# Optimization experiments

Hardware: AMD Instinct MI355X
Metric: run time of the kernel (lower is better)

## Reference

```python
import jax, jax.numpy as jnp
import numpy as np

VOCAB = 32000
H = 256        # d_model
L = 4096       # l_max
N = 64         # SSM state size (S4 default)
CH = 1         # channels
BATCH = 8
PAD = 0        # pad_token_id
DT_MIN, DT_MAX = 0.001, 0.1


def setup_inputs() -> dict:
    key = jax.random.key(0)
    ks = jax.random.split(key, 8)
    input_ids = jax.random.randint(ks[0], (BATCH, L), 0, VOCAB)
    embedding = (jax.random.normal(ks[1], (VOCAB, H), dtype=jnp.float32) * 0.02).at[PAD].set(0.0)
    # S4D-Lin style initialization
    log_dt = jnp.log(DT_MIN) + jax.random.uniform(ks[2], (H,), dtype=jnp.float32) * (np.log(DT_MAX) - np.log(DT_MIN))
    A_log_re = jnp.full((H, N), np.log(0.5), dtype=jnp.float32)          # A_real = -exp(A_log_re)
    A_im = jnp.broadcast_to(np.pi * jnp.arange(N, dtype=jnp.float32), (H, N)).copy()
    B_re = jnp.ones((H, N), dtype=jnp.float32)
    B_im = jnp.zeros((H, N), dtype=jnp.float32)
    # bidirectional => 2*CH output channels for C
    C_re = jax.random.normal(ks[3], (2 * CH, H, N), dtype=jnp.float32) * (0.5 ** 0.5)
    C_im = jax.random.normal(ks[4], (2 * CH, H, N), dtype=jnp.float32) * (0.5 ** 0.5)
    D = jax.random.normal(ks[5], (CH, H), dtype=jnp.float32)
    W_out = jax.random.normal(ks[6], (2 * H, CH * H), dtype=jnp.float32) / np.sqrt(CH * H)
    b_out = jnp.zeros((2 * H,), dtype=jnp.float32)
    return {"input_ids": input_ids, "embedding": embedding, "log_dt": log_dt,
            "A_log_re": A_log_re, "A_im": A_im, "B_re": B_re, "B_im": B_im,
            "C_re": C_re, "C_im": C_im, "D": D, "W_out": W_out, "b_out": b_out}


def _s4_forward(input_ids, embedding, log_dt, A_log_re, A_im, B_re, B_im, C_re, C_im, D, W_out, b_out):
    u = embedding[input_ids]                 # (B, L, H) embedding lookup
    u = jnp.swapaxes(u, 1, 2)                # (B, H, L) transposed=True
    dt = jnp.exp(log_dt)                     # (H,)
    A = -jnp.exp(A_log_re) + 1j * A_im       # (H, N) Hurwitz diagonal SSM
    dtA = dt[:, None] * A                    # (H, N)
    dA = jnp.exp(dtA)                        # discrete A (ZOH)
    dB = (B_re + 1j * B_im) * (dA - 1.0) / A # discrete B (ZOH), (H, N)
    Cc = C_re + 1j * C_im                    # (2*CH, H, N)
    # Vandermonde kernel: K[c,h,l] = 2*Re(sum_n C[c,h,n] dB[h,n] exp(dtA[h,n]*l))
    pos = jnp.arange(L, dtype=jnp.float32)
    vand = jnp.exp(dtA[:, :, None] * pos)    # (H, N, L) complex
    K = 2.0 * jnp.einsum('chn,hn,hnl->chl', Cc, dB, vand).real  # (2*CH, H, L)
    # bidirectional: causal kernel + flipped anti-causal kernel, conv length 2L
    k0, k1 = K[:CH], K[CH:]
    k = jnp.pad(k0, ((0, 0), (0, 0), (0, L))) + jnp.pad(k1[..., ::-1], ((0, 0), (0, 0), (L, 0)))
    k_f = jnp.fft.rfft(k, n=2 * L)           # (CH, H, L+1)
    u_f = jnp.fft.rfft(u, n=2 * L)           # (B, H, L+1)
    y = jnp.fft.irfft(u_f[:, None] * k_f[None], n=2 * L)[..., :L]  # (B, CH, H, L)
    y = y + u[:, None, :, :] * D[None, :, :, None]                 # skip connection
    y = y.reshape(u.shape[0], CH * H, L)
    y = jax.nn.gelu(y, approximate=False)
    z = jnp.einsum('oi,bil->bol', W_out, y) + b_out[None, :, None]  # (B, 2H, L)
    y = z[:, :H] * jax.nn.sigmoid(z[:, H:])                          # GLU
    y = jnp.swapaxes(y, 1, 2)                # (B, L, H)
    return y[:, -1]                           # pool='last' -> (B, H)


def reference(input_ids, embedding, log_dt, A_log_re, A_im, B_re, B_im, C_re, C_im, D, W_out, b_out):
    return _s4_forward(input_ids, embedding, log_dt, A_log_re, A_im, B_re, B_im, C_re, C_im, D, W_out, b_out)
```

## Files before the change

### kernel.cpp

```cpp
#include <hip/hip_runtime.h>
#include <math.h>

#define HH 256
#define NN 64
#define LL 4096
#define BB 8


__global__ __launch_bounds__(512) void frontend_kernel(
    const int* __restrict__ ids, const float* __restrict__ emb,
    const float* __restrict__ log_dt, const float* __restrict__ A_log_re,
    const float* __restrict__ A_im, const float* __restrict__ B_re,
    const float* __restrict__ B_im, const float* __restrict__ C_re,
    const float* __restrict__ C_im,
    float* __restrict__ u_ws, float* __restrict__ Krev) {
    __shared__ union {
        struct { int ids_s[64]; float tb[2][64][65]; } a;
        struct { float powR[64][65]; float powI[64][65];
                 float2 dAt[64]; float2 e64t[64]; float2 W2[8][64]; } k;
    } sm;
    int t = threadIdx.x;
    if (blockIdx.x < BB * 64) {
        int b = blockIdx.x >> 6;
        int tile = blockIdx.x & 63;
        int w = t >> 6;
        int lane = t & 63;
        int rq = lane >> 4;
        int k = lane & 15;
        if (t < 64) sm.a.ids_s[t] = ids[b * LL + tile * 64 + t];
        __syncthreads();
        {
            int r0 = w * 8 + rq;
            float4 v0 = *(const float4*)(emb + (long)sm.a.ids_s[r0] * HH + 4 * k);
            float4 v1 = *(const float4*)(emb + (long)sm.a.ids_s[r0 + 4] * HH + 4 * k);
            sm.a.tb[0][r0][4 * k + 0] = v0.x;
            sm.a.tb[0][r0][4 * k + 1] = v0.y;
            sm.a.tb[0][r0][4 * k + 2] = v0.z;
            sm.a.tb[0][r0][4 * k + 3] = v0.w;
            sm.a.tb[0][r0 + 4][4 * k + 0] = v1.x;
            sm.a.tb[0][r0 + 4][4 * k + 1] = v1.y;
            sm.a.tb[0][r0 + 4][4 * k + 2] = v1.z;
            sm.a.tb[0][r0 + 4][4 * k + 3] = v1.w;
        }
        __syncthreads();
        #pragma unroll
        for (int c4 = 0; c4 < 4; ++c4) {
            int cur = c4 & 1;
            float4 v0, v1;
            if (c4 < 3) {
                int r0 = w * 8 + rq;
                v0 = *(const float4*)(emb + (long)sm.a.ids_s[r0] * HH +
                                      (c4 + 1) * 64 + 4 * k);
                v1 = *(const float4*)(emb + (long)sm.a.ids_s[r0 + 4] * HH +
                                      (c4 + 1) * 64 + 4 * k);
            }
            #pragma unroll
            for (int it = 0; it < 2; ++it) {
                int hq = w * 8 + it * 4 + rq;
                int s0 = 4 * k;
                float4 o;
                o.x = sm.a.tb[cur][s0 + 0][hq];
                o.y = sm.a.tb[cur][s0 + 1][hq];
                o.z = sm.a.tb[cur][s0 + 2][hq];
                o.w = sm.a.tb[cur][s0 + 3][hq];
                *(float4*)(u_ws + ((long)(b * HH + c4 * 64 + hq)) * LL +
                           tile * 64 + s0) = o;
            }
            if (c4 < 3) {
                int r0 = w * 8 + rq;
                sm.a.tb[cur ^ 1][r0][4 * k + 0] = v0.x;
                sm.a.tb[cur ^ 1][r0][4 * k + 1] = v0.y;
                sm.a.tb[cur ^ 1][r0][4 * k + 2] = v0.z;
                sm.a.tb[cur ^ 1][r0][4 * k + 3] = v0.w;
                sm.a.tb[cur ^ 1][r0 + 4][4 * k + 0] = v1.x;
                sm.a.tb[cur ^ 1][r0 + 4][4 * k + 1] = v1.y;
                sm.a.tb[cur ^ 1][r0 + 4][4 * k + 2] = v1.z;
                sm.a.tb[cur ^ 1][r0 + 4][4 * k + 3] = v1.w;
            }
            __syncthreads();
        }
    } else {
        int h = blockIdx.x - BB * 64;
        int w = __builtin_amdgcn_readfirstlane(t >> 6);
        int lane = t & 63;
        if (t < NN) {
            int n = t;
            int idx = h * NN + n;
            float dt = expf(log_dt[h]);
            float Are = -expf(A_log_re[idx]);
            float Aim = A_im[idx];
            float ea = expf(dt * Are);
            float sn, cs;
            sincosf(dt * Aim, &sn, &cs);
            float dAre = ea * cs, dAim = ea * sn;
            float numre = dAre - 1.0f, numim = dAim;
            float den = Are * Are + Aim * Aim;
            float qre = (numre * Are + numim * Aim) / den;
            float qim = (numim * Are - numre * Aim) / den;
            float bre = B_re[idx], bim = B_im[idx];
            float dBre = bre * qre - bim * qim;
            float dBim = bre * qim + bim * qre;
            float cre = C_re[idx], cim = C_im[idx];
            float wre = 2.0f * (cre * dBre - cim * dBim);
            float wim = 2.0f * (cre * dBim + cim * dBre);
            sm.k.dAt[n] = make_float2(dAre, dAim);
            float pr = dAre, pi = dAim;
            #pragma unroll
            for (int kq = 0; kq < 6; ++kq) {
                float nr = pr * pr - pi * pi;
                pi = 2.0f * pr * pi; pr = nr;
            }
            sm.k.e64t[n] = make_float2(pr, pi);
            #pragma unroll
            for (int kq = 0; kq < 3; ++kq) {
                float nr = pr * pr - pi * pi;
                pi = 2.0f * pr * pi; pr = nr;
            }
            float qr2 = wre, qi2 = wim;
            #pragma unroll
            for (int kk = 0; kk < 8; ++kk) {
                sm.k.W2[kk][n] = make_float2(qr2, qi2);
                float nr = qr2 * pr - qi2 * pi, ni = qr2 * pi + qi2 * pr;
                qr2 = nr; qi2 = ni;
            }
        }
        __syncthreads();
        {
            float2 a = sm.k.dAt[lane];
            float br = a.x, bi = a.y;
            #pragma unroll
            for (int kq = 0; kq < 3; ++kq) {
                float nr = br * br - bi * bi;
                bi = 2.0f * br * bi; br = nr;
            }
            float pr = 1.0f, pi = 0.0f;
            #pragma unroll
            for (int bit = 0; bit < 3; ++bit) {
                if ((w >> bit) & 1) {
                    float tr = pr * br - pi * bi;
                    pi = pr * bi + pi * br; pr = tr;
                }
                float t2 = br * br - bi * bi;
                bi = 2.0f * br * bi; br = t2;
            }
            #pragma unroll
            for (int i = 0; i < 8; ++i) {
                sm.k.powR[8 * w + i][lane] = pr;
                sm.k.powI[8 * w + i][lane] = pi;
                float tr = pr * a.x - pi * a.y;
                pi = pr * a.y + pi * a.x; pr = tr;
            }
        }
        __syncthreads();
        float kacc[8];
        #pragma unroll
        for (int j = 0; j < 8; ++j) kacc[j] = 0.0f;
        #pragma unroll 2
        for (int n = 0; n < NN; ++n) {
            float Pr = sm.k.powR[lane][n];
            float Pi = sm.k.powI[lane][n];
            float2 E = sm.k.e64t[n];
            float2 Wn = sm.k.W2[w][n];
            float vr = Wn.x * Pr - Wn.y * Pi;
            float vi = Wn.x * Pi + Wn.y * Pr;
            #pragma unroll
            for (int j = 0; j < 8; ++j) {
                kacc[j] += vr;
                float tr = vr * E.x - vi * E.y;
                vi = vr * E.y + vi * E.x; vr = tr;
            }
        }
        #pragma unroll
        for (int j = 0; j < 8; ++j) {
            int l = w * 512 + j * 64 + lane;
            Krev[h * LL + (LL - 1 - l)] = kacc[j];
        }
    }
}

__global__ __launch_bounds__(256) void conv_kernel(
    const float* __restrict__ u_ws, const float* __restrict__ Krev,
    const float* __restrict__ Dv, float* __restrict__ g) {
    __shared__ float partial[4];
    int t = threadIdx.x;
    int bh = blockIdx.x;
    int h = bh & (HH - 1);
    const float4* up = (const float4*)(u_ws + (long)bh * LL);
    const float4* kp = (const float4*)(Krev + h * LL);
    float acc = 0.0f;
    #pragma unroll
    for (int i = 0; i < 4; ++i) {
        float4 uv = up[i * 256 + t];
        float4 kv = kp[i * 256 + t];
        acc += uv.x * kv.x + uv.y * kv.y + uv.z * kv.z + uv.w * kv.w;
    }
    #pragma unroll
    for (int m = 32; m > 0; m >>= 1) acc += __shfl_xor(acc, m);
    if ((t & 63) == 0) partial[t >> 6] = acc;
    __syncthreads();
    if (t == 0) {
        float y = partial[0] + partial[1] + partial[2] + partial[3]
                + u_ws[(long)bh * LL + LL - 1] * Dv[h];
        float ge = 0.5f * y * (1.0f + erff(y * 0.70710678118654752f));
        g[bh] = ge;
    }
}

__global__ __launch_bounds__(256) void out_kernel(
    const float* __restrict__ g, const float* __restrict__ W,
    const float* __restrict__ bvec, float* __restrict__ out) {
    int b = blockIdx.x >> 7;
    int tile = blockIdx.x & 127;
    int t = threadIdx.x;
    int w = t >> 6, lane = t & 63;
    __shared__ float gs[HH];
    __shared__ float zb[4];
    gs[t] = g[b * HH + t];
    __syncthreads();
    int hh = tile * 2 + (w >> 1);
    int o = (w & 1) * HH + hh;
    float4 wv4 = ((const float4*)(W + o * HH))[lane];
    float4 gv4 = ((const float4*)gs)[lane];
    float p = wv4.x * gv4.x + wv4.y * gv4.y + wv4.z * gv4.z + wv4.w * gv4.w;
    #pragma unroll
    for (int m = 32; m > 0; m >>= 1) p += __shfl_xor(p, m);
    if (lane == 0) zb[w] = p + bvec[o];
    __syncthreads();
    if (t < 2) {
        int hq = tile * 2 + t;
        float z1 = zb[t * 2 + 0];
        float z2 = zb[t * 2 + 1];
        out[b * HH + hq] = z1 * (1.0f / (1.0f + expf(-z2)));
    }
}

extern "C" void kernel_launch(void* const* d_in, const int* in_sizes, int n_in,
                              void* d_out, int out_size, void* d_ws, size_t ws_size,
                              hipStream_t stream) {
    const int* input_ids = (const int*)d_in[0];
    const float* embedding = (const float*)d_in[1];
    const float* log_dt = (const float*)d_in[2];
    const float* A_log_re = (const float*)d_in[3];
    const float* A_im = (const float*)d_in[4];
    const float* B_re = (const float*)d_in[5];
    const float* B_im = (const float*)d_in[6];
    const float* C_re = (const float*)d_in[7];
    const float* C_im = (const float*)d_in[8];
    const float* D = (const float*)d_in[9];
    const float* W_out = (const float*)d_in[10];
    const float* b_out = (const float*)d_in[11];
    float* out = (float*)d_out;

    float* ws = (float*)d_ws;
    float* u_ws = ws + 327680;
    float* g = ws + 10813440;
    float* Krev = ws + 10815488;

    frontend_kernel<<<BB * 64 + HH, 512, 0, stream>>>(
        input_ids, embedding, log_dt, A_log_re, A_im, B_re, B_im, C_re, C_im,
        u_ws, Krev);

    conv_kernel<<<BB * HH, 256, 0, stream>>>(u_ws, Krev, D, g);

    out_kernel<<<BB * 128, 256, 0, stream>>>(g, W_out, b_out, out);
}
```

Baseline: 119.4 us.

## Gather embeddings directly in conv instead of materializing transposed u

Removes the separate embedding-gather-and-transpose pass that wrote the full (B,H,L) activation tensor to workspace. The K kernel is now stored time-major, and a new conv kernel gathers embedding rows by token id, multiplying them against K tiles loaded into LDS through async global-to-LDS loads, then writes per-chunk partial sums. The output kernel reduces those partials and fuses the skip term, GELU, projection and GLU, using one block per batch element. This cuts a large intermediate write and re-read, in exchange for a serialized K-generation stage ahead of the conv and a small grid in the final kernel.

```diff
diff --git a/kernel.cpp b/kernel.cpp
--- a/kernel.cpp
+++ b/kernel.cpp
@@ -5,232 +5,196 @@
 #define NN 64
 #define LL 4096
 #define BB 8
-
-
-__global__ __launch_bounds__(512) void frontend_kernel(
-    const int* __restrict__ ids, const float* __restrict__ emb,
+#define TK 32
+#define NCH (LL / TK)
+
+
+__global__ __launch_bounds__(512) void kmat_kernel(
     const float* __restrict__ log_dt, const float* __restrict__ A_log_re,
     const float* __restrict__ A_im, const float* __restrict__ B_re,
     const float* __restrict__ B_im, const float* __restrict__ C_re,
-    const float* __restrict__ C_im,
-    float* __restrict__ u_ws, float* __restrict__ Krev) {
-    __shared__ union {
-        struct { int ids_s[64]; float tb[2][64][65]; } a;
-        struct { float powR[64][65]; float powI[64][65];
-                 float2 dAt[64]; float2 e64t[64]; float2 W2[8][64]; } k;
-    } sm;
+    const float* __restrict__ C_im, float* __restrict__ Ktrev) {
+    __shared__ struct {
+        float powR[64][65]; float powI[64][65];
+        float2 dAt[64]; float2 e64t[64]; float2 W2[8][64];
+    } sk;
     int t = threadIdx.x;
-    if (blockIdx.x < BB * 64) {
-        int b = blockIdx.x >> 6;
-        int tile = blockIdx.x & 63;
-        int w = t >> 6;
-        int lane = t & 63;
-        int rq = lane >> 4;
-        int k = lane & 15;
-        if (t < 64) sm.a.ids_s[t] = ids[b * LL + tile * 64 + t];
-        __syncthreads();
-        {
-            int r0 = w * 8 + rq;
-            float4 v0 = *(const float4*)(emb + (long)sm.a.ids_s[r0] * HH + 4 * k);
-            float4 v1 = *(const float4*)(emb + (long)sm.a.ids_s[r0 + 4] * HH + 4 * k);
-            sm.a.tb[0][r0][4 * k + 0] = v0.x;
-            sm.a.tb[0][r0][4 * k + 1] = v0.y;
-            sm.a.tb[0][r0][4 * k + 2] = v0.z;
-            sm.a.tb[0][r0][4 * k + 3] = v0.w;
-            sm.a.tb[0][r0 + 4][4 * k + 0] = v1.x;
-            sm.a.tb[0][r0 + 4][4 * k + 1] = v1.y;
-            sm.a.tb[0][r0 + 4][4 * k + 2] = v1.z;
-            sm.a.tb[0][r0 + 4][4 * k + 3] = v1.w;
-        }
-        __syncthreads();
-        #pragma unroll
-        for (int c4 = 0; c4 < 4; ++c4) {
-            int cur = c4 & 1;
-            float4 v0, v1;
-            if (c4 < 3) {
-                int r0 = w * 8 + rq;
-                v0 = *(const float4*)(emb + (long)sm.a.ids_s[r0] * HH +
-                                      (c4 + 1) * 64 + 4 * k);
-                v1 = *(const float4*)(emb + (long)sm.a.ids_s[r0 + 4] * HH +
-                                      (c4 + 1) * 64 + 4 * k);
+    int h = blockIdx.x;
+    int w = __builtin_amdgcn_readfirstlane(t >> 6);
+    int lane = t & 63;
+    if (t < NN) {
+        int n = t;
+        int idx = h * NN + n;
+        float dt = expf(log_dt[h]);
+        float Are = -expf(A_log_re[idx]);
+        float Aim = A_im[idx];
+        float ea = expf(dt * Are);
+        float sn, cs;
+        sincosf(dt * Aim, &sn, &cs);
+        float dAre = ea * cs, dAim = ea * sn;
+        float numre = dAre - 1.0f, numim = dAim;
+        float den = Are * Are + Aim * Aim;
+        float qre = (numre * Are + numim * Aim) / den;
+        float qim = (numim * Are - numre * Aim) / den;
+        float bre = B_re[idx], bim = B_im[idx];
+        float dBre = bre * qre - bim * qim;
+        float dBim = bre * qim + bim * qre;
+        float cre = C_re[idx], cim = C_im[idx];
+        float wre = 2.0f * (cre * dBre - cim * dBim);
+        float wim = 2.0f * (cre * dBim + cim * dBre);
+        sk.dAt[n] = make_float2(dAre, dAim);
+        float pr = dAre, pi = dAim;
+        #pragma unroll
+        for (int kq = 0; kq < 6; ++kq) {
+            float nr = pr * pr - pi * pi;
+            pi = 2.0f * pr * pi; pr = nr;
+        }
+        sk.e64t[n] = make_float2(pr, pi);
+        #pragma unroll
+        for (int kq = 0; kq < 3; ++kq) {
+            float nr = pr * pr - pi * pi;
+            pi = 2.0f * pr * pi; pr = nr;
+        }
+        float qr2 = wre, qi2 = wim;
+        #pragma unroll
+        for (int kk = 0; kk < 8; ++kk) {
+            sk.W2[kk][n] = make_float2(qr2, qi2);
+            float nr = qr2 * pr - qi2 * pi, ni = qr2 * pi + qi2 * pr;
+            qr2 = nr; qi2 = ni;
+        }
+    }
+    __syncthreads();
+    {
+        float2 a = sk.dAt[lane];
+        float br = a.x, bi = a.y;
+        #pragma unroll
+        for (int kq = 0; kq < 3; ++kq) {
+            float nr = br * br - bi * bi;
+            bi = 2.0f * br * bi; br = nr;
+        }
+        float pr = 1.0f, pi = 0.0f;
+        #pragma unroll
+        for (int bit = 0; bit < 3; ++bit) {
+            if ((w >> bit) & 1) {
+                float tr = pr * br - pi * bi;
+                pi = pr * bi + pi * br; pr = tr;
             }
-            #pragma unroll
-            for (int it = 0; it < 2; ++it) {
-                int hq = w * 8 + it * 4 + rq;
-                int s0 = 4 * k;
-                float4 o;
-                o.x = sm.a.tb[cur][s0 + 0][hq];
-                o.y = sm.a.tb[cur][s0 + 1][hq];
-                o.z = sm.a.tb[cur][s0 + 2][hq];
-                o.w = sm.a.tb[cur][s0 + 3][hq];
-                *(float4*)(u_ws + ((long)(b * HH + c4 * 64 + hq)) * LL +
-                           tile * 64 + s0) = o;
-            }
-            if (c4 < 3) {
-                int r0 = w * 8 + rq;
-                sm.a.tb[cur ^ 1][r0][4 * k + 0] = v0.x;
-                sm.a.tb[cur ^ 1][r0][4 * k + 1] = v0.y;
-                sm.a.tb[cur ^ 1][r0][4 * k + 2] = v0.z;
-                sm.a.tb[cur ^ 1][r0][4 * k + 3] = v0.w;
-                sm.a.tb[cur ^ 1][r0 + 4][4 * k + 0] = v1.x;
-                sm.a.tb[cur ^ 1][r0 + 4][4 * k + 1] = v1.y;
-                sm.a.tb[cur ^ 1][r0 + 4][4 * k + 2] = v1.z;
-                sm.a.tb[cur ^ 1][r0 + 4][4 * k + 3] = v1.w;
-            }
-            __syncthreads();
-        }
-    } else {
-        int h = blockIdx.x - BB * 64;
-        int w = __builtin_amdgcn_readfirstlane(t >> 6);
-        int lane = t & 63;
-        if (t < NN) {
-            int n = t;
-            int idx = h * NN + n;
-            float dt = expf(log_dt[h]);
-            float Are = -expf(A_log_re[idx]);
-            float Aim = A_im[idx];
-            float ea = expf(dt * Are);
-            float sn, cs;
-            sincosf(dt * Aim, &sn, &cs);
-            float dAre = ea * cs, dAim = ea * sn;
-            float numre = dAre - 1.0f, numim = dAim;
-            float den = Are * Are + Aim * Aim;
-            float qre = (numre * Are + numim * Aim) / den;
-            float qim = (numim * Are - numre * Aim) / den;
-            float bre = B_re[idx], bim = B_im[idx];
-            float dBre = bre * qre - bim * qim;
-            float dBim = bre * qim + bim * qre;
-            float cre = C_re[idx], cim = C_im[idx];
-            float wre = 2.0f * (cre * dBre - cim * dBim);
-            float wim = 2.0f * (cre * dBim + cim * dBre);
-            sm.k.dAt[n] = make_float2(dAre, dAim);
-            float pr = dAre, pi = dAim;
-            #pragma unroll
-            for (int kq = 0; kq < 6; ++kq) {
-                float nr = pr * pr - pi * pi;
-                pi = 2.0f * pr * pi; pr = nr;
-            }
-            sm.k.e64t[n] = make_float2(pr, pi);
-            #pragma unroll
-            for (int kq = 0; kq < 3; ++kq) {
-                float nr = pr * pr - pi * pi;
-                pi = 2.0f * pr * pi; pr = nr;
-            }
-            float qr2 = wre, qi2 = wim;
-            #pragma unroll
-            for (int kk = 0; kk < 8; ++kk) {
-                sm.k.W2[kk][n] = make_float2(qr2, qi2);
-                float nr = qr2 * pr - qi2 * pi, ni = qr2 * pi + qi2 * pr;
-                qr2 = nr; qi2 = ni;
-            }
-        }
-        __syncthreads();
-        {
-            float2 a = sm.k.dAt[lane];
-            float br = a.x, bi = a.y;
-            #pragma unroll
-            for (int kq = 0; kq < 3; ++kq) {
-                float nr = br * br - bi * bi;
-                bi = 2.0f * br * bi; br = nr;
-            }
-            float pr = 1.0f, pi = 0.0f;
-            #pragma unroll
-            for (int bit = 0; bit < 3; ++bit) {
-                if ((w >> bit) & 1) {
-                    float tr = pr * br - pi * bi;
-                    pi = pr * bi + pi * br; pr = tr;
-                }
-                float t2 = br * br - bi * bi;
-                bi = 2.0f * br * bi; br = t2;
-            }
-            #pragma unroll
-            for (int i = 0; i < 8; ++i) {
-                sm.k.powR[8 * w + i][lane] = pr;
-                sm.k.powI[8 * w + i][lane] = pi;
-                float tr = pr * a.x - pi * a.y;
-                pi = pr * a.y + pi * a.x; pr = tr;
-            }
-        }
-        __syncthreads();
-        float kacc[8];
-        #pragma unroll
-        for (int j = 0; j < 8; ++j) kacc[j] = 0.0f;
-        #pragma unroll 2
-        for (int n = 0; n < NN; ++n) {
-            float Pr = sm.k.powR[lane][n];
-            float Pi = sm.k.powI[lane][n];
-            float2 E = sm.k.e64t[n];
-            float2 Wn = sm.k.W2[w][n];
-            float vr = Wn.x * Pr - Wn.y * Pi;
-            float vi = Wn.x * Pi + Wn.y * Pr;
-            #pragma unroll
-            for (int j = 0; j < 8; ++j) {
-                kacc[j] += vr;
-                float tr = vr * E.x - vi * E.y;
-                vi = vr * E.y + vi * E.x; vr = tr;
-            }
-        }
+            float t2 = br * br - bi * bi;
+            bi = 2.0f * br * bi; br = t2;
+        }
+        #pragma unroll
+        for (int i = 0; i < 8; ++i) {
+            sk.powR[8 * w + i][lane] = pr;
+            sk.powI[8 * w + i][lane] = pi;
+            float tr = pr * a.x - pi * a.y;
+            pi = pr * a.y + pi * a.x; pr = tr;
+        }
+    }
+    __syncthreads();
+    float kacc[8];
+    #pragma unroll
+    for (int j = 0; j < 8; ++j) kacc[j] = 0.0f;
+    #pragma unroll 2
+    for (int n = 0; n < NN; ++n) {
+        float Pr = sk.powR[lane][n];
+        float Pi = sk.powI[lane][n];
+        float2 E = sk.e64t[n];
+        float2 Wn = sk.W2[w][n];
+        float vr = Wn.x * Pr - Wn.y * Pi;
+        float vi = Wn.x * Pi + Wn.y * Pr;
         #pragma unroll
         for (int j = 0; j < 8; ++j) {
-            int l = w * 512 + j * 64 + lane;
-            Krev[h * LL + (LL - 1 - l)] = kacc[j];
-        }
-    }
-}
-
-__global__ __launch_bounds__(256) void conv_kernel(
-    const float* __restrict__ u_ws, const float* __restrict__ Krev,
-    const float* __restrict__ Dv, float* __restrict__ g) {
-    __shared__ float partial[4];
+            kacc[j] += vr;
+            float tr = vr * E.x - vi * E.y;
+            vi = vr * E.y + vi * E.x; vr = tr;
+        }
+    }
+    #pragma unroll
+    for (int j = 0; j < 8; ++j) {
+        int l = w * 512 + j * 64 + lane;
+        Ktrev[(long)(LL - 1 - l) * HH + h] = kacc[j];
+    }
+}
+
+__global__ __launch_bounds__(256) void gconv_kernel(
+    const int* __restrict__ ids, const float* __restrict__ emb,
+    const float* __restrict__ Ktrev, float* __restrict__ ypart) {
+    __shared__ float Kls[TK * HH];
+    __shared__ int idsl[TK];
     int t = threadIdx.x;
-    int bh = blockIdx.x;
-    int h = bh & (HH - 1);
-    const float4* up = (const float4*)(u_ws + (long)bh * LL);
-    const float4* kp = (const float4*)(Krev + h * LL);
+    int b = blockIdx.x >> 7;
+    int c = blockIdx.x & (NCH - 1);
+    int i0 = c * TK;
+    int wv = t >> 6, lane = t & 63;
+    if (t < TK) idsl[t] = ids[b * LL + i0 + t];
+    {
+        const float* src = Ktrev + (long)i0 * HH;
+        #pragma unroll
+        for (int r = 0; r < 8; ++r) {
+            int row = wv * 8 + r;
+            __builtin_amdgcn_global_load_lds(
+                (const __attribute__((address_space(1))) void*)
+                    (src + row * HH + lane * 4),
+                (__attribute__((address_space(3))) void*)(&Kls[row * HH]),
+                16, 0, 0);
+        }
+    }
+    __syncthreads();
     float acc = 0.0f;
-    #pragma unroll
-    for (int i = 0; i < 4; ++i) {
-        float4 uv = up[i * 256 + t];
-        float4 kv = kp[i * 256 + t];
-        acc += uv.x * kv.x + uv.y * kv.y + uv.z * kv.z + uv.w * kv.w;
-    }
-    #pragma unroll
-    for (int m = 32; m > 0; m >>= 1) acc += __shfl_xor(acc, m);
-    if ((t & 63) == 0) partial[t >> 6] = acc;
-    __syncthreads();
-    if (t == 0) {
-        float y = partial[0] + partial[1] + partial[2] + partial[3]
-                + u_ws[(long)bh * LL + LL - 1] * Dv[h];
-        float ge = 0.5f * y * (1.0f + erff(y * 0.70710678118654752f));
-        g[bh] = ge;
-    }
-}
-
-__global__ __launch_bounds__(256) void out_kernel(
-    const float* __restrict__ g, const float* __restrict__ W,
-    const float* __restrict__ bvec, float* __restrict__ out) {
-    int b = blockIdx.x >> 7;
-    int tile = blockIdx.x & 127;
+    #pragma unroll 8
+    for (int l = 0; l < TK; ++l) {
+        int id = idsl[l];
+        float v = emb[(long)id * HH + t];
+        acc = fmaf(v, Kls[l * HH + t], acc);
+    }
+    ypart[((long)(b * NCH + c)) * HH + t] = acc;
+}
+
+__global__ __launch_bounds__(512) void out_kernel(
+    const float* __restrict__ ypart, const int* __restrict__ ids,
+    const float* __restrict__ emb, const float* __restrict__ Dv,
+    const float* __restrict__ W, const float* __restrict__ bvec,
+    float* __restrict__ out) {
+    __shared__ float red[8][HH];
+    __shared__ float gs[HH];
+    __shared__ float zb[2 * HH];
     int t = threadIdx.x;
-    int w = t >> 6, lane = t & 63;
-    __shared__ float gs[HH];
-    __shared__ float zb[4];
-    gs[t] = g[b * HH + t];
-    __syncthreads();
-    int hh = tile * 2 + (w >> 1);
-    int o = (w & 1) * HH + hh;
-    float4 wv4 = ((const float4*)(W + o * HH))[lane];
-    float4 gv4 = ((const float4*)gs)[lane];
-    float p = wv4.x * gv4.x + wv4.y * gv4.y + wv4.z * gv4.z + wv4.w * gv4.w;
-    #pragma unroll
-    for (int m = 32; m > 0; m >>= 1) p += __shfl_xor(p, m);
-    if (lane == 0) zb[w] = p + bvec[o];
-    __syncthreads();
-    if (t < 2) {
-        int hq = tile * 2 + t;
-        float z1 = zb[t * 2 + 0];
-        float z2 = zb[t * 2 + 1];
-        out[b * HH + hq] = z1 * (1.0f / (1.0f + expf(-z2)));
+    int b = blockIdx.x;
+    int wv = t >> 6, lane = t & 63;
+    float4 s4 = make_float4(0.f, 0.f, 0.f, 0.f);
+    const float4* yp4 = (const float4*)(ypart + (long)b * NCH * HH);
+    #pragma unroll 4
+    for (int cc = 0; cc < 16; ++cc) {
+        float4 v = yp4[(wv * 16 + cc) * 64 + lane];
+        s4.x += v.x; s4.y += v.y; s4.z += v.z; s4.w += v.w;
+    }
+    *(float4*)&red[wv][lane * 4] = s4;
+    __syncthreads();
+    if (t < HH) {
+        float s = 0.0f;
+        #pragma unroll
+        for (int w2 = 0; w2 < 8; ++w2) s += red[w2][t];
+        int idl = ids[b * LL + LL - 1];
+        float ul = emb[(long)idl * HH + t];
+        float y = s + ul * Dv[t];
+        gs[t] = 0.5f * y * (1.0f + erff(y * 0.70710678118654752f));
+    }
+    __syncthreads();
+    #pragma unroll 2
+    for (int oo = 0; oo < 64; ++oo) {
+        int o = wv * 64 + oo;
+        float4 wr = ((const float4*)(W + o * HH))[lane];
+        float4 gr = ((const float4*)gs)[lane];
+        float p = wr.x * gr.x + wr.y * gr.y + wr.z * gr.z + wr.w * gr.w;
+        #pragma unroll
+        for (int m = 32; m > 0; m >>= 1) p += __shfl_xor(p, m);
+        if (lane == 0) zb[o] = p + bvec[o];
+    }
+    __syncthreads();
+    if (t < HH) {
+        float z1 = zb[t];
+        float z2 = zb[t + HH];
+        out[b * HH + t] = z1 * (1.0f / (1.0f + expf(-z2)));
     }
 }
 
@@ -252,15 +216,15 @@
     float* out = (float*)d_out;
 
     float* ws = (float*)d_ws;
-    float* u_ws = ws + 327680;
-    float* g = ws + 10813440;
-    float* Krev = ws + 10815488;
-
-    frontend_kernel<<<BB * 64 + HH, 512, 0, stream>>>(
-        input_ids, embedding, log_dt, A_log_re, A_im, B_re, B_im, C_re, C_im,
-        u_ws, Krev);
-
-    conv_kernel<<<BB * HH, 256, 0, stream>>>(u_ws, Krev, D, g);
-
-    out_kernel<<<BB * 128, 256, 0, stream>>>(g, W_out, b_out, out);
-}
+    float* Ktrev = ws;
+    float* ypart = ws + 1048576;
+
+    kmat_kernel<<<HH, 512, 0, stream>>>(
+        log_dt, A_log_re, A_im, B_re, B_im, C_re, C_im, Ktrev);
+
+    gconv_kernel<<<BB * NCH, 256, 0, stream>>>(
+        input_ids, embedding, Ktrev, ypart);
+
+    out_kernel<<<BB, 512, 0, stream>>>(
+        ypart, input_ids, embedding, D, W_out, b_out, out);
+}
```

New measurement: 158.9 us. 33.1% more time.
